# Kernel tuning notes

Hardware: AMD Instinct MI355X
Metric: run time of the kernel (lower is better)

## Reference

```python
import jax, jax.numpy as jnp
from jax import lax
import numpy as np

DEPTH, D_MODEL, D_INNER, D_STATE, DT_RANK = 24, 192, 384, 16, 12
EPS = 1e-5

def _layernorm(x, w, b):
    m = x.mean(-1, keepdims=True)
    v = ((x - m) ** 2).mean(-1, keepdims=True)
    return (x - m) * lax.rsqrt(v + EPS) * w + b

def _silu(x):
    return x * jax.nn.sigmoid(x)

def _mamba_mixer(x, in_w, cw, cb, xp_w, dtw, dtb, a_log, dvec, out_w):
    # x: (B, L, D_MODEL)
    B, L, _ = x.shape
    xz = jnp.einsum('bld,ed->ble', x, in_w)            # (B, L, 2*D_INNER)
    xi, z = xz[..., :D_INNER], xz[..., D_INNER:]
    # causal depthwise conv1d, kernel 4 (left-pad 3, truncate to L)
    xt = jnp.moveaxis(xi, 1, 2)                        # (B, D_INNER, L)
    xt = jnp.pad(xt, ((0, 0), (0, 0), (3, 0)))
    xt = lax.conv_general_dilated(xt, cw[:, None, :], (1,), 'VALID',
                                  dimension_numbers=('NCH', 'OIH', 'NCH'),
                                  feature_group_count=D_INNER)
    xt = _silu(xt + cb[None, :, None])
    xc = jnp.moveaxis(xt, 1, 2)                        # (B, L, D_INNER)
    x_dbl = jnp.einsum('bld,ed->ble', xc, xp_w)        # (B, L, DT_RANK+2*D_STATE)
    dt = x_dbl[..., :DT_RANK]
    Bm = x_dbl[..., DT_RANK:DT_RANK + D_STATE]         # (B, L, N)
    Cm = x_dbl[..., DT_RANK + D_STATE:]                # (B, L, N)
    delta = jax.nn.softplus(jnp.einsum('blr,dr->bld', dt, dtw) + dtb)  # (B, L, D_INNER)
    A = -jnp.exp(a_log)                                # (D_INNER, N)
    dA = jnp.exp(delta[..., None] * A)                 # (B, L, D_INNER, N)
    dBx = (delta * xc)[..., None] * Bm[:, :, None, :]  # (B, L, D_INNER, N)

    def step(h, inp):
        dA_t, dBx_t, C_t = inp
        h = dA_t * h + dBx_t
        y = jnp.einsum('bdn,bn->bd', h, C_t)
        return h, y

    h0 = jnp.zeros((B, D_INNER, D_STATE), x.dtype)
    _, ys = lax.scan(step, h0, (jnp.moveaxis(dA, 1, 0), jnp.moveaxis(dBx, 1, 0), jnp.moveaxis(Cm, 1, 0)))
    y = jnp.moveaxis(ys, 0, 1) + xc * dvec             # (B, L, D_INNER)
    y = y * _silu(z)
    return jnp.einsum('ble,de->bld', y, out_w)

def _forward(x, patch_w, patch_b, norm_w, norm_b, in_proj_w, conv_w, conv_b,
             x_proj_w, dt_w, dt_b, A_log, Dp, out_proj_w, normf_w, normf_b, head_w, head_b):
    # patch embed: conv 16x16 stride 16 -> (B, 192, 14, 14) -> (B, 196, 192)
    h = lax.conv_general_dilated(x, patch_w, (16, 16), 'VALID',
                                 dimension_numbers=('NCHW', 'OIHW', 'NCHW'))
    h = h + patch_b[None, :, None, None]
    B = h.shape[0]
    hidden = h.reshape(B, D_MODEL, -1).transpose(0, 2, 1)  # (B, L, D)
    residual = None
    for d in range(DEPTH):
        residual = hidden if residual is None else residual + hidden
        normed = _layernorm(residual, norm_w[d], norm_b[d])
        hidden = _mamba_mixer(normed, in_proj_w[d], conv_w[d], conv_b[d], x_proj_w[d],
                              dt_w[d], dt_b[d], A_log[d], Dp[d], out_proj_w[d])
    residual = residual + hidden
    feat = _layernorm(residual, normf_w, normf_b)
    pooled = feat.mean(axis=1)                           # final_pool_type='mean'
    return pooled @ head_w.T + head_b                    # (B, num_classes)

def setup_inputs() -> dict:
    key = jax.random.key(0)
    ks = jax.random.split(key, 16)
    s = 0.05
    return {
        'x': jax.random.normal(ks[0], (64, 3, 224, 224), jnp.float32),
        'patch_w': jax.random.normal(ks[1], (192, 3, 16, 16), jnp.float32) * s,
        'patch_b': jnp.zeros((192,), jnp.float32),
        'norm_w': jnp.ones((DEPTH, D_MODEL), jnp.float32),
        'norm_b': jnp.zeros((DEPTH, D_MODEL), jnp.float32),
        'in_proj_w': jax.random.normal(ks[2], (DEPTH, 2 * D_INNER, D_MODEL), jnp.float32) * s,
        'conv_w': jax.random.normal(ks[3], (DEPTH, D_INNER, 4), jnp.float32) * 0.3,
        'conv_b': jnp.zeros((DEPTH, D_INNER), jnp.float32),
        'x_proj_w': jax.random.normal(ks[4], (DEPTH, DT_RANK + 2 * D_STATE, D_INNER), jnp.float32) * s,
        'dt_w': jax.random.normal(ks[5], (DEPTH, D_INNER, DT_RANK), jnp.float32) * s,
        'dt_b': jax.random.uniform(ks[6], (DEPTH, D_INNER), jnp.float32, -4.0, -2.0),
        'A_log': jnp.log(jnp.broadcast_to(jnp.arange(1, D_STATE + 1, dtype=jnp.float32), (DEPTH, D_INNER, D_STATE))),
        'Dp': jnp.ones((DEPTH, D_INNER), jnp.float32),
        'out_proj_w': jax.random.normal(ks[7], (DEPTH, D_MODEL, D_INNER), jnp.float32) * s,
        'normf_w': jnp.ones((D_MODEL,), jnp.float32),
        'normf_b': jnp.zeros((D_MODEL,), jnp.float32),
        'head_w': jax.random.normal(ks[8], (1000, D_MODEL), jnp.float32) * s,
        'head_b': jnp.zeros((1000,), jnp.float32),
    }

def reference(x, patch_w, patch_b, norm_w, norm_b, in_proj_w, conv_w, conv_b,
              x_proj_w, dt_w, dt_b, A_log, Dp, out_proj_w, normf_w, normf_b, head_w, head_b):
    return _forward(x, patch_w, patch_b, norm_w, norm_b, in_proj_w, conv_w, conv_b,
                    x_proj_w, dt_w, dt_b, A_log, Dp, out_proj_w, normf_w, normf_b, head_w, head_b)
```

## Files before the change

kernel.cpp:

```cpp
#include <hip/hip_runtime.h>
#include <math.h>


#define DEPTH 24
#define DM 192
#define DI 384
#define DS 16
#define DR 12
#define SEQL 196
#define BATCH 64
#define MROWS (BATCH*SEQL)
#define XDP 8624
#define LOG2E 1.44269504088896340736f

typedef unsigned short ushort_t;
typedef __bf16 bf16x8 __attribute__((ext_vector_type(8)));
typedef float f32x4 __attribute__((ext_vector_type(4)));

__device__ __forceinline__ float sigmoidf_(float x) { return 1.f / (1.f + __expf(-x)); }

__device__ __forceinline__ ushort_t f2bf(float f) {
    union { float f; unsigned u; } c; c.f = f;
    unsigned u = c.u;
    return (ushort_t)((u + 0x7FFFu + ((u >> 16) & 1u)) >> 16);
}
__device__ __forceinline__ float bf2f(ushort_t u) {
    union { unsigned u; float f; } c; c.u = ((unsigned)u) << 16;
    return c.f;
}

__device__ __forceinline__ void load_lds16(const ushort_t* g, ushort_t* l) {
    __builtin_amdgcn_global_load_lds((__attribute__((address_space(1))) void*)g,
                                     (__attribute__((address_space(3))) void*)l, 16, 0, 0);
}

template<int CTRL>
__device__ __forceinline__ float dpp_mov(float oldv, float src) {
    return __builtin_bit_cast(float, __builtin_amdgcn_update_dpp(
        __builtin_bit_cast(int, oldv), __builtin_bit_cast(int, src),
        CTRL, 0xF, 0xF, false));
}

__device__ __forceinline__ float row16_sum(float v) {
    v += dpp_mov<0xB1>(0.f, v);
    v += dpp_mov<0x4E>(0.f, v);
    v += dpp_mov<0x141>(0.f, v);
    v += dpp_mov<0x140>(0.f, v);
    return v;
}

__global__ void f2bf4_kernel(const float* __restrict__ src, ushort_t* __restrict__ dst, int n4) {
    int i = blockIdx.x * 256 + threadIdx.x;
    if (i >= n4) return;
    float4 v = ((const float4*)src)[i];
    union { ushort_t s[4]; uint2 u; } o;
    o.s[0] = f2bf(v.x); o.s[1] = f2bf(v.y); o.s[2] = f2bf(v.z); o.s[3] = f2bf(v.w);
    ((uint2*)dst)[i] = o.u;
}

__global__ void xp_pad_kernel(const float* __restrict__ src, ushort_t* __restrict__ dst) {
    int i = blockIdx.x * 256 + threadIdx.x;
    if (i >= DEPTH * 64 * 384) return;
    int col = i % 384, row = (i / 384) & 63, d = i / (384 * 64);
    float v = (row < 44) ? src[(size_t)d * 44 * 384 + row * 384 + col] : 0.f;
    dst[i] = f2bf(v);
}

template<bool BF>
__global__ void ln_kernel(float* __restrict__ residual, const float* __restrict__ hidden,
                          const float* __restrict__ w, const float* __restrict__ b,
                          void* __restrict__ out_) {
    int wave = threadIdx.x >> 6, lane = threadIdx.x & 63;
    int row = blockIdx.x * 4 + wave;
    float* rr = residual + (size_t)row * DM;
    const float* hr = hidden + (size_t)row * DM;
    float v0 = rr[lane]       + hr[lane];
    float v1 = rr[lane + 64]  + hr[lane + 64];
    float v2 = rr[lane + 128] + hr[lane + 128];
    rr[lane] = v0; rr[lane + 64] = v1; rr[lane + 128] = v2;
    float s = v0 + v1 + v2;
    #pragma unroll
    for (int off = 32; off > 0; off >>= 1) s += __shfl_down(s, off);
    float mean = __shfl(s, 0) * (1.f / DM);
    float d0 = v0 - mean, d1 = v1 - mean, d2 = v2 - mean;
    float q = d0 * d0 + d1 * d1 + d2 * d2;
    #pragma unroll
    for (int off = 32; off > 0; off >>= 1) q += __shfl_down(q, off);
    float rstd = rsqrtf(__shfl(q, 0) * (1.f / DM) + 1e-5f);
    float o0 = d0 * rstd * w[lane]       + b[lane];
    float o1 = d1 * rstd * w[lane + 64]  + b[lane + 64];
    float o2 = d2 * rstd * w[lane + 128] + b[lane + 128];
    if constexpr (BF) {
        ushort_t* o = (ushort_t*)out_ + (size_t)row * DM;
        o[lane] = f2bf(o0); o[lane + 64] = f2bf(o1); o[lane + 128] = f2bf(o2);
    } else {
        float* o = (float*)out_ + (size_t)row * DM;
        o[lane] = o0; o[lane + 64] = o1; o[lane + 128] = o2;
    }
}

template<int BN, int WM, int WN, int NST, bool TC>
__global__ __launch_bounds__(256, 2) void gemm_mfma(const ushort_t* __restrict__ A,
        const ushort_t* __restrict__ W, float* __restrict__ C, int K, int ldC) {
    constexpr int FM = 128 / (WM * 16);
    constexpr int FN = BN / (WN * 16);
    __shared__ ushort_t sA[128 * 32];
    __shared__ ushort_t sB[BN * 32];
    const int t = threadIdx.x;
    const int wave = t >> 6, lane = t & 63;
    const int lr = lane & 15, lq = lane >> 4;
    const int wr = wave / WN, wc = wave % WN;
    const int m0 = blockIdx.x * 128, n0 = blockIdx.y * BN;
    const int wbase = t & ~63;

    f32x4 acc[FM][FN];
    #pragma unroll
    for (int i = 0; i < FM; i++)
        #pragma unroll
        for (int j = 0; j < FN; j++) acc[i][j] = f32x4{0.f, 0.f, 0.f, 0.f};

    for (int k0 = 0; k0 < K; k0 += 32) {
        __syncthreads();
        #pragma unroll
        for (int c = 0; c < 2; c++) {
            int s = c * 256 + t;
            int row = s >> 2;
            int quad = (s & 3) ^ ((row >> 1) & 3);
            load_lds16(A + (size_t)(m0 + row) * K + k0 + quad * 8,
                       sA + (size_t)(c * 256 + wbase) * 8);
        }
        #pragma unroll
        for (int c = 0; c < BN * 4 / 256; c++) {
            int s = c * 256 + t;
            int row = s >> 2;
            int quad = (s & 3) ^ ((row >> 1) & 3);
            load_lds16(W + (size_t)(n0 + row) * K + k0 + quad * 8,
                       sB + (size_t)(c * 256 + wbase) * 8);
        }
        __syncthreads();
        bf16x8 af[FM], bfr[FN];
        #pragma unroll
        for (int i = 0; i < FM; i++) {
            int row = wr * FM * 16 + i * 16 + lr;
            int slot = (row << 2) | (lq ^ ((row >> 1) & 3));
            af[i] = *(const bf16x8*)&sA[(size_t)slot * 8];
        }
        #pragma unroll
        for (int j = 0; j < FN; j++) {
            int row = wc * FN * 16 + j * 16 + lr;
            int slot = (row << 2) | (lq ^ ((row >> 1) & 3));
            bfr[j] = *(const bf16x8*)&sB[(size_t)slot * 8];
        }
        #pragma unroll
        for (int i = 0; i < FM; i++)
            #pragma unroll
            for (int j = 0; j < FN; j++)
                acc[i][j] = __builtin_amdgcn_mfma_f32_16x16x32_bf16(af[i], bfr[j], acc[i][j], 0, 0, 0);
    }
    int crow0 = m0 + wr * FM * 16 + lq * 4;
    int ccol0 = n0 + wc * FN * 16 + lr;
    if constexpr (TC) {
        #pragma unroll
        for (int i = 0; i < FM; i++) {
            int m = crow0 + i * 16;
            int bb = m / 196, l = m % 196;
            #pragma unroll
            for (int j = 0; j < FN; j++) {
                int col = ccol0 + j * 16;
                if (col < 44) {
                    float4 v = {acc[i][j][0], acc[i][j][1], acc[i][j][2], acc[i][j][3]};
                    *(float4*)(C + (size_t)bb * XDP + (size_t)col * 196 + l) = v;
                }
            }
        }
    } else {
        #pragma unroll
        for (int i = 0; i < FM; i++)
            #pragma unroll
            for (int j = 0; j < FN; j++) {
                if (wc * FN + j >= NST) continue;
                float* cp = C + (size_t)(crow0 + i * 16) * ldC + ccol0 + j * 16;
                #pragma unroll
                for (int r = 0; r < 4; r++) cp[(size_t)r * ldC] = acc[i][j][r];
            }
    }
}

__global__ __launch_bounds__(256, 2) void gemm_patch_mfma(const ushort_t* __restrict__ Xbf,
        const ushort_t* __restrict__ Wbf, const float* __restrict__ bias, float* __restrict__ C) {
    constexpr int FM = 2, FN = 4;
    __shared__ ushort_t sA[128 * 32];
    __shared__ ushort_t sB[64 * 32];
    const int t = threadIdx.x;
    const int wave = t >> 6, lane = t & 63;
    const int lr = lane & 15, lq = lane >> 4;
    const int m0 = blockIdx.x * 128, n0 = blockIdx.y * 64;
    const int wbase = t & ~63;

    const ushort_t* abase[2];
    int aquad[2];
    #pragma unroll
    for (int c = 0; c < 2; c++) {
        int s = c * 256 + t;
        int row = s >> 2;
        aquad[c] = (s & 3) ^ ((row >> 1) & 3);
        int m = m0 + row;
        int b = m / 196, r = m % 196, py = r / 14, px = r % 14;
        abase[c] = Xbf + (size_t)b * 150528 + py * 3584 + px * 16;
    }
    int brow = t >> 2;
    int bquad = (t & 3) ^ ((brow >> 1) & 3);
    const ushort_t* bbase = Wbf + (size_t)(n0 + brow) * 768 + bquad * 8;

    f32x4 acc[FM][FN];
    #pragma unroll
    for (int i = 0; i < FM; i++)
        #pragma unroll
        for (int j = 0; j < FN; j++) acc[i][j] = f32x4{0.f, 0.f, 0.f, 0.f};

    for (int k0 = 0; k0 < 768; k0 += 32) {
        __syncthreads();
        #pragma unroll
        for (int c = 0; c < 2; c++) {
            int k = k0 + aquad[c] * 8;
            int ci = k >> 8, ky = (k >> 4) & 15, kx0 = k & 15;
            load_lds16(abase[c] + ci * 50176 + ky * 224 + kx0,
                       sA + (size_t)(c * 256 + wbase) * 8);
        }
        load_lds16(bbase + k0, sB + (size_t)wbase * 8);
        __syncthreads();
        bf16x8 af[FM], bfr[FN];
        #pragma unroll
        for (int i = 0; i < FM; i++) {
            int row = wave * FM * 16 + i * 16 + lr;
            int slot = (row << 2) | (lq ^ ((row >> 1) & 3));
            af[i] = *(const bf16x8*)&sA[(size_t)slot * 8];
        }
        #pragma unroll
        for (int j = 0; j < FN; j++) {
            int row = j * 16 + lr;
            int slot = (row << 2) | (lq ^ ((row >> 1) & 3));
            bfr[j] = *(const bf16x8*)&sB[(size_t)slot * 8];
        }
        #pragma unroll
        for (int i = 0; i < FM; i++)
            #pragma unroll
            for (int j = 0; j < FN; j++)
                acc[i][j] = __builtin_amdgcn_mfma_f32_16x16x32_bf16(af[i], bfr[j], acc[i][j], 0, 0, 0);
    }
    int crow0 = m0 + wave * FM * 16 + lq * 4;
    int ccol0 = n0 + lr;
    #pragma unroll
    for (int i = 0; i < FM; i++)
        #pragma unroll
        for (int j = 0; j < FN; j++) {
            int col = ccol0 + j * 16;
            float bv = bias[col];
            float* cp = C + (size_t)(crow0 + i * 16) * DM + col;
            #pragma unroll
            for (int r = 0; r < 4; r++) cp[(size_t)r * DM] = acc[i][j][r] + bv;
        }
}

template<bool BIAS>
__global__ __launch_bounds__(256, 2) void gemm64(const float* __restrict__ A,
        const float* __restrict__ W, const float* __restrict__ bias,
        float* __restrict__ C, int M, int N, int K) {
    __shared__ float As[32][68];
    __shared__ float Ws[32][68];
    int t = threadIdx.x;
    int m0 = blockIdx.x * 64, n0 = blockIdx.y * 64;
    int lr = t >> 2, lk = (t & 3) * 4;
    int am = m0 + lr; bool avld = am < M;
    const float* Ap = A + (size_t)(avld ? am : 0) * K + lk;
    int wn = n0 + lr; bool wv = wn < N;
    const float* Wp = W + (size_t)(wv ? wn : 0) * K + lk;
    int tm = (t >> 4) * 4, tn = (t & 15) * 4;
    float acc[4][4];
    #pragma unroll
    for (int i = 0; i < 4; i++)
        #pragma unroll
        for (int j = 0; j < 4; j++) acc[i][j] = 0.f;

    for (int k0 = 0; k0 < K; k0 += 32) {
        float4 a0 = make_float4(0.f, 0.f, 0.f, 0.f), a1 = a0, w0 = a0, w1 = a0;
        if (avld) { a0 = *(const float4*)(Ap + k0); a1 = *(const float4*)(Ap + k0 + 16); }
        if (wv)   { w0 = *(const float4*)(Wp + k0); w1 = *(const float4*)(Wp + k0 + 16); }
        __syncthreads();
        As[lk + 0][lr] = a0.x; As[lk + 1][lr] = a0.y; As[lk + 2][lr] = a0.z; As[lk + 3][lr] = a0.w;
        As[lk + 16][lr] = a1.x; As[lk + 17][lr] = a1.y; As[lk + 18][lr] = a1.z; As[lk + 19][lr] = a1.w;
        Ws[lk + 0][lr] = w0.x; Ws[lk + 1][lr] = w0.y; Ws[lk + 2][lr] = w0.z; Ws[lk + 3][lr] = w0.w;
        Ws[lk + 16][lr] = w1.x; Ws[lk + 17][lr] = w1.y; Ws[lk + 18][lr] = w1.z; Ws[lk + 19][lr] = w1.w;
        __syncthreads();
        #pragma unroll
        for (int kk = 0; kk < 32; kk++) {
            float4 x0 = *(const float4*)&As[kk][tm];
            float4 y0 = *(const float4*)&Ws[kk][tn];
            float av[4] = {x0.x, x0.y, x0.z, x0.w};
            float bv[4] = {y0.x, y0.y, y0.z, y0.w};
            #pragma unroll
            for (int i = 0; i < 4; i++)
                #pragma unroll
                for (int j = 0; j < 4; j++) acc[i][j] = fmaf(av[i], bv[j], acc[i][j]);
        }
    }
    #pragma unroll
    for (int i = 0; i < 4; i++) {
        int m = m0 + tm + i;
        if (m >= M) continue;
        float* cr = C + (size_t)m * N;
        int n = n0 + tn;
        if (n < N) {
            float4 v = {acc[i][0], acc[i][1], acc[i][2], acc[i][3]};
            if (BIAS) { v.x += bias[n]; v.y += bias[n + 1]; v.z += bias[n + 2]; v.w += bias[n + 3]; }
            *(float4*)(cr + n) = v;
        }
    }
}

__global__ void conv_silu_kernel(const float* __restrict__ xz, const float* __restrict__ cw,
                                 const float* __restrict__ cb, ushort_t* __restrict__ xcbf) {
    int idx = blockIdx.x * 256 + threadIdx.x;
    if (idx >= MROWS * DI) return;
    int e = idx % DI; int bl = idx / DI; int l = bl % SEQL; int b = bl / SEQL;
    const float* base = xz + (size_t)(b * SEQL) * 768 + e;
    float w0 = cw[e * 4], w1 = cw[e * 4 + 1], w2 = cw[e * 4 + 2], w3 = cw[e * 4 + 3];
    float acc = cb[e];
    if (l >= 3) acc = fmaf(base[(size_t)(l - 3) * 768], w0, acc);
    if (l >= 2) acc = fmaf(base[(size_t)(l - 2) * 768], w1, acc);
    if (l >= 1) acc = fmaf(base[(size_t)(l - 1) * 768], w2, acc);
    acc = fmaf(base[(size_t)l * 768], w3, acc);
    xcbf[idx] = f2bf(acc * sigmoidf_(acc));
}

__global__ __launch_bounds__(512, 6) void scan_kernel(const float* __restrict__ xdt,
        const ushort_t* __restrict__ xcbf, const float* __restrict__ xz,
        const float* __restrict__ dtw, const float* __restrict__ dtb,
        const float* __restrict__ a_log, const float* __restrict__ Dp, ushort_t* __restrict__ y) {
    __shared__ float sd[44 * 196];
    __shared__ float dls[8][196];
    __shared__ float dus[8][196];
    __shared__ ushort_t xcs[8 * 196];
    const int b = blockIdx.x, eg = blockIdx.y;
    const int tid = threadIdx.x;
    const int wave = tid >> 6, lane = tid & 63;
    const int e = eg * 8 + wave;
    const int n = lane & 15, c = lane >> 4;

    {
        const float4* src4 = (const float4*)(xdt + (size_t)b * XDP);
        float4* sd4 = (float4*)sd;
        for (int i = tid; i < XDP / 4; i += 512) sd4[i] = src4[i];
    }
    float wv = 0.f;
    if (lane < DR) wv = dtw[(size_t)e * DR + lane];
    float4 zr0 = make_float4(0.f, 0.f, 0.f, 0.f), zr1 = zr0;
    if (tid < 196) {
        int l = tid;
        const ushort_t* xp = xcbf + (size_t)(b * SEQL + l) * DI + eg * 8;
        ushort4 xq0 = *(const ushort4*)xp;
        ushort4 xq1 = *(const ushort4*)(xp + 4);
        const float* zp = xz + (size_t)(b * SEQL + l) * 768 + DI + eg * 8;
        zr0 = *(const float4*)zp;
        zr1 = *(const float4*)(zp + 4);
        xcs[0 * 196 + l] = xq0.x; xcs[1 * 196 + l] = xq0.y;
        xcs[2 * 196 + l] = xq0.z; xcs[3 * 196 + l] = xq0.w;
        xcs[4 * 196 + l] = xq1.x; xcs[5 * 196 + l] = xq1.y;
        xcs[6 * 196 + l] = xq1.z; xcs[7 * 196 + l] = xq1.w;
    }
    __syncthreads();

    const float Avn = -__expf(a_log[(size_t)e * DS + n]) * LOG2E;
    const float db = dtb[e];
    const bool act = lane < 49;
    const int lb = act ? lane * 4 : 0;

    if (act) {
        f32x4 dt4 = {db, db, db, db};
        #pragma unroll
        for (int k = 0; k < DR; k++) {
            f32x4 r = *(const f32x4*)&sd[k * 196 + lb];
            dt4 += r * __shfl(wv, k);
        }
        f32x4 d4;
        #pragma unroll
        for (int s = 0; s < 4; s++) {
            float v = dt4[s];
            d4[s] = (v > 20.f) ? v : __logf(1.f + __expf(v));
        }
        ushort4 xcq = *(const ushort4*)&xcs[wave * 196 + lb];
        f32x4 du4 = d4 * f32x4{bf2f(xcq.x), bf2f(xcq.y), bf2f(xcq.z), bf2f(xcq.w)};
        *(f32x4*)&dls[wave][lb] = d4;
        *(f32x4*)&dus[wave][lb] = du4;
    }

    const int t0 = (c == 0) ? 0 : 48 * c + 4;
    const int iters = (c == 0) ? 13 : 12;
    const float* Brow = &sd[(12 + n) * 196];
    const float* Crow = &sd[(28 + n) * 196];
    const float* dlw = dls[wave];
    const float* duw = dus[wave];

    float h = 0.f;
    f32x4 dsum = {0.f, 0.f, 0.f, 0.f};
    for (int i = 0; i < iters; i++) {
        int t = t0 + 4 * i;
        f32x4 dl = *(const f32x4*)&dlw[t];
        f32x4 du = *(const f32x4*)&duw[t];
        f32x4 Bn = *(const f32x4*)&Brow[t];
        dsum += dl;
        #pragma unroll
        for (int s = 0; s < 4; s++) {
            float dA = __builtin_amdgcn_exp2f(dl[s] * Avn);
            h = fmaf(h, dA, du[s] * Bn[s]);
        }
    }
    float P = __builtin_amdgcn_exp2f(Avn * (dsum[0] + dsum[1] + dsum[2] + dsum[3]));

    {
        float hp = __shfl_up(h, 16), pp = __shfl_up(P, 16);
        if (c >= 1) { h = fmaf(P, hp, h); P *= pp; }
        hp = __shfl_up(h, 32); pp = __shfl_up(P, 32);
        if (c >= 2) { h = fmaf(P, hp, h); P *= pp; }
    }
    float hin = __shfl_up(h, 16);
    if (c == 0) hin = 0.f;

    const float Dv = Dp[e];
    ushort_t* xcw = &xcs[wave * 196];
    h = hin;
    for (int i = 0; i < iters; i++) {
        int t = t0 + 4 * i;
        f32x4 dl = *(const f32x4*)&dlw[t];
        f32x4 du = *(const f32x4*)&duw[t];
        f32x4 Bn = *(const f32x4*)&Brow[t];
        f32x4 Cn = *(const f32x4*)&Crow[t];
        f32x4 yp;
        #pragma unroll
        for (int s = 0; s < 4; s++) {
            float dA = __builtin_amdgcn_exp2f(dl[s] * Avn);
            h = fmaf(h, dA, du[s] * Bn[s]);
            yp[s] = h * Cn[s];
        }
        #pragma unroll
        for (int s = 0; s < 4; s++) yp[s] = row16_sum(yp[s]);
        if (n < 4) {
            float ysel = (n == 0) ? yp[0] : (n == 1) ? yp[1] : (n == 2) ? yp[2] : yp[3];
            float xcsel = bf2f(xcw[t + n]);
            xcw[t + n] = f2bf(fmaf(xcsel, Dv, ysel));
        }
    }
    __syncthreads();
    if (tid < 196) {
        int l = tid;
        float zv[8] = {zr0.x, zr0.y, zr0.z, zr0.w, zr1.x, zr1.y, zr1.z, zr1.w};
        union { ushort_t s[8]; ushort4 q[2]; } o;
        #pragma unroll
        for (int k = 0; k < 8; k++) {
            float yv = bf2f(xcs[k * 196 + l]);
            float z = zv[k];
            o.s[k] = f2bf(yv * z * sigmoidf_(z));
        }
        ushort_t* yp = y + (size_t)(b * SEQL + l) * DI + eg * 8;
        *(ushort4*)yp = o.q[0];
        *(ushort4*)(yp + 4) = o.q[1];
    }
}

__global__ void pool_kernel(const float* __restrict__ normed, float* __restrict__ pooled) {
    int b = blockIdx.x, d = threadIdx.x;
    float s = 0.f;
    for (int l = 0; l < SEQL; l++) s += normed[(size_t)(b * SEQL + l) * DM + d];
    pooled[b * DM + d] = s * (1.f / 196.f);
}

extern "C" void kernel_launch(void* const* d_in, const int* in_sizes, int n_in,
                              void* d_out, int out_size, void* d_ws, size_t ws_size,
                              hipStream_t stream) {
    const float* x       = (const float*)d_in[0];
    const float* patch_w = (const float*)d_in[1];
    const float* patch_b = (const float*)d_in[2];
    const float* norm_w  = (const float*)d_in[3];
    const float* norm_b  = (const float*)d_in[4];
    const float* in_w    = (const float*)d_in[5];
    const float* conv_w  = (const float*)d_in[6];
    const float* conv_b  = (const float*)d_in[7];
    const float* xp_w    = (const float*)d_in[8];
    const float* dt_w    = (const float*)d_in[9];
    const float* dt_b    = (const float*)d_in[10];
    const float* A_log   = (const float*)d_in[11];
    const float* Dp      = (const float*)d_in[12];
    const float* out_w   = (const float*)d_in[13];
    const float* normf_w = (const float*)d_in[14];
    const float* normf_b = (const float*)d_in[15];
    const float* head_w  = (const float*)d_in[16];
    const float* head_b  = (const float*)d_in[17];

    float* ws = (float*)d_ws;
    float* residual     = ws;
    float* hidden       = ws + 2408448;
    float* xz           = ws + 4816896;
    ushort_t* xcbf      = (ushort_t*)(ws + 14450688);
    ushort_t* y_bf      = (ushort_t*)(ws + 16859136);
    ushort_t* x_bf      = (ushort_t*)(ws + 14450688);
    ushort_t* normed_bf = (ushort_t*)(ws + 19267584);
    float* xdbl_t       = ws + 20471808;
    float* pooled       = ws + 21023744;
    ushort_t* in_w_bf   = (ushort_t*)(ws + 21036032);
    ushort_t* out_w_bf  = (ushort_t*)(ws + 22805504);
    ushort_t* xp_w_bf   = (ushort_t*)(ws + 23690240);
    ushort_t* patch_w_bf= (ushort_t*)(ws + 23985152);

    (void)hipMemsetAsync(residual, 0, (size_t)2408448 * sizeof(float), stream);

    f2bf4_kernel<<<3456, 256, 0, stream>>>(in_w, in_w_bf, 884736);
    f2bf4_kernel<<<1728, 256, 0, stream>>>(out_w, out_w_bf, 442368);
    f2bf4_kernel<<<144, 256, 0, stream>>>(patch_w, patch_w_bf, 36864);
    f2bf4_kernel<<<9408, 256, 0, stream>>>(x, x_bf, 2408448);
    xp_pad_kernel<<<2304, 256, 0, stream>>>(xp_w, xp_w_bf);

    gemm_patch_mfma<<<dim3(98, 3), 256, 0, stream>>>(x_bf, patch_w_bf, patch_b, hidden);

    for (int d = 0; d < DEPTH; ++d) {
        ln_kernel<true><<<3136, 256, 0, stream>>>(residual, hidden, norm_w + d * DM,
                                                  norm_b + d * DM, normed_bf);
        gemm_mfma<192, 2, 2, 12, false><<<dim3(98, 4), 256, 0, stream>>>(normed_bf,
                in_w_bf + (size_t)d * 768 * 192, xz, 192, 768);
        conv_silu_kernel<<<18816, 256, 0, stream>>>(xz, conv_w + d * DI * 4, conv_b + d * DI, xcbf);
        gemm_mfma<64, 4, 1, 3, true><<<dim3(98, 1), 256, 0, stream>>>(xcbf,
                xp_w_bf + (size_t)d * 64 * 384, xdbl_t, 384, 196);
        scan_kernel<<<dim3(64, 48), 512, 0, stream>>>(xdbl_t, xcbf, xz, dt_w + d * DI * DR,
                dt_b + d * DI, A_log + d * DI * DS, Dp + d * DI, y_bf);
        gemm_mfma<64, 4, 1, 4, false><<<dim3(98, 3), 256, 0, stream>>>(y_bf,
                out_w_bf + (size_t)d * 192 * 384, hidden, 384, 192);
    }

    ln_kernel<false><<<3136, 256, 0, stream>>>(residual, hidden, normf_w, normf_b, xz);
    pool_kernel<<<64, 192, 0, stream>>>(xz, pooled);
    gemm64<true><<<dim3(1, 16), 256, 0, stream>>>(pooled, head_w, head_b, (float*)d_out, 64, 1000, 192);
}
```

Baseline: 3.030 ms.

## Fuse residual add into out_proj GEMM, vectorize conv, shrink GEMM M tiles

Accumulates the out_proj result directly into the residual buffer in the GEMM epilogue. LayerNorm then only reads the residual, which removes the separate hidden buffer, the residual write-back and the initial memset. The causal conv+SiLU kernel now processes four channels per thread with float4 loads. The x_proj and out_proj GEMMs use 64-row tiles to launch twice as many blocks. The read-modify-write epilogue adds a load of C per output element.

```diff
diff --git a/kernel.cpp b/kernel.cpp
--- a/kernel.cpp
+++ b/kernel.cpp
@@ -67,17 +67,15 @@
 }
 
 template<bool BF>
-__global__ void ln_kernel(float* __restrict__ residual, const float* __restrict__ hidden,
+__global__ void ln_kernel(const float* __restrict__ residual,
                           const float* __restrict__ w, const float* __restrict__ b,
                           void* __restrict__ out_) {
     int wave = threadIdx.x >> 6, lane = threadIdx.x & 63;
     int row = blockIdx.x * 4 + wave;
-    float* rr = residual + (size_t)row * DM;
-    const float* hr = hidden + (size_t)row * DM;
-    float v0 = rr[lane]       + hr[lane];
-    float v1 = rr[lane + 64]  + hr[lane + 64];
-    float v2 = rr[lane + 128] + hr[lane + 128];
-    rr[lane] = v0; rr[lane + 64] = v1; rr[lane + 128] = v2;
+    const float* rr = residual + (size_t)row * DM;
+    float v0 = rr[lane];
+    float v1 = rr[lane + 64];
+    float v2 = rr[lane + 128];
     float s = v0 + v1 + v2;
     #pragma unroll
     for (int off = 32; off > 0; off >>= 1) s += __shfl_down(s, off);
@@ -99,18 +97,18 @@
     }
 }
 
-template<int BN, int WM, int WN, int NST, bool TC>
+template<int BM, int BN, int WM, int WN, int NST, bool TC, bool RESADD>
 __global__ __launch_bounds__(256, 2) void gemm_mfma(const ushort_t* __restrict__ A,
         const ushort_t* __restrict__ W, float* __restrict__ C, int K, int ldC) {
-    constexpr int FM = 128 / (WM * 16);
+    constexpr int FM = BM / (WM * 16);
     constexpr int FN = BN / (WN * 16);
-    __shared__ ushort_t sA[128 * 32];
+    __shared__ ushort_t sA[BM * 32];
     __shared__ ushort_t sB[BN * 32];
     const int t = threadIdx.x;
     const int wave = t >> 6, lane = t & 63;
     const int lr = lane & 15, lq = lane >> 4;
     const int wr = wave / WN, wc = wave % WN;
-    const int m0 = blockIdx.x * 128, n0 = blockIdx.y * BN;
+    const int m0 = blockIdx.x * BM, n0 = blockIdx.y * BN;
     const int wbase = t & ~63;
 
     f32x4 acc[FM][FN];
@@ -122,7 +120,7 @@
     for (int k0 = 0; k0 < K; k0 += 32) {
         __syncthreads();
         #pragma unroll
-        for (int c = 0; c < 2; c++) {
+        for (int c = 0; c < BM * 4 / 256; c++) {
             int s = c * 256 + t;
             int row = s >> 2;
             int quad = (s & 3) ^ ((row >> 1) & 3);
@@ -181,7 +179,10 @@
                 if (wc * FN + j >= NST) continue;
                 float* cp = C + (size_t)(crow0 + i * 16) * ldC + ccol0 + j * 16;
                 #pragma unroll
-                for (int r = 0; r < 4; r++) cp[(size_t)r * ldC] = acc[i][j][r];
+                for (int r = 0; r < 4; r++) {
+                    if constexpr (RESADD) cp[(size_t)r * ldC] += acc[i][j][r];
+                    else                  cp[(size_t)r * ldC]  = acc[i][j][r];
+                }
             }
     }
 }
@@ -321,16 +322,34 @@
 __global__ void conv_silu_kernel(const float* __restrict__ xz, const float* __restrict__ cw,
                                  const float* __restrict__ cb, ushort_t* __restrict__ xcbf) {
     int idx = blockIdx.x * 256 + threadIdx.x;
-    if (idx >= MROWS * DI) return;
-    int e = idx % DI; int bl = idx / DI; int l = bl % SEQL; int b = bl / SEQL;
-    const float* base = xz + (size_t)(b * SEQL) * 768 + e;
-    float w0 = cw[e * 4], w1 = cw[e * 4 + 1], w2 = cw[e * 4 + 2], w3 = cw[e * 4 + 3];
-    float acc = cb[e];
-    if (l >= 3) acc = fmaf(base[(size_t)(l - 3) * 768], w0, acc);
-    if (l >= 2) acc = fmaf(base[(size_t)(l - 2) * 768], w1, acc);
-    if (l >= 1) acc = fmaf(base[(size_t)(l - 1) * 768], w2, acc);
-    acc = fmaf(base[(size_t)l * 768], w3, acc);
-    xcbf[idx] = f2bf(acc * sigmoidf_(acc));
+    if (idx >= MROWS * (DI / 4)) return;
+    int eq = idx % (DI / 4); int bl = idx / (DI / 4);
+    int l = bl % SEQL; int b = bl / SEQL;
+    int e4 = eq * 4;
+    const float* base = xz + (size_t)(b * SEQL) * 768 + e4;
+    float4 wa = *(const float4*)(cw + (e4 + 0) * 4);
+    float4 wb = *(const float4*)(cw + (e4 + 1) * 4);
+    float4 wc = *(const float4*)(cw + (e4 + 2) * 4);
+    float4 wd = *(const float4*)(cw + (e4 + 3) * 4);
+    float4 acc = *(const float4*)(cb + e4);
+    if (l >= 3) { float4 xv = *(const float4*)(base + (size_t)(l - 3) * 768);
+        acc.x = fmaf(xv.x, wa.x, acc.x); acc.y = fmaf(xv.y, wb.x, acc.y);
+        acc.z = fmaf(xv.z, wc.x, acc.z); acc.w = fmaf(xv.w, wd.x, acc.w); }
+    if (l >= 2) { float4 xv = *(const float4*)(base + (size_t)(l - 2) * 768);
+        acc.x = fmaf(xv.x, wa.y, acc.x); acc.y = fmaf(xv.y, wb.y, acc.y);
+        acc.z = fmaf(xv.z, wc.y, acc.z); acc.w = fmaf(xv.w, wd.y, acc.w); }
+    if (l >= 1) { float4 xv = *(const float4*)(base + (size_t)(l - 1) * 768);
+        acc.x = fmaf(xv.x, wa.z, acc.x); acc.y = fmaf(xv.y, wb.z, acc.y);
+        acc.z = fmaf(xv.z, wc.z, acc.z); acc.w = fmaf(xv.w, wd.z, acc.w); }
+    { float4 xv = *(const float4*)(base + (size_t)l * 768);
+        acc.x = fmaf(xv.x, wa.w, acc.x); acc.y = fmaf(xv.y, wb.w, acc.y);
+        acc.z = fmaf(xv.z, wc.w, acc.z); acc.w = fmaf(xv.w, wd.w, acc.w); }
+    ushort4 o;
+    o.x = f2bf(acc.x * sigmoidf_(acc.x));
+    o.y = f2bf(acc.y * sigmoidf_(acc.y));
+    o.z = f2bf(acc.z * sigmoidf_(acc.z));
+    o.w = f2bf(acc.w * sigmoidf_(acc.w));
+    *(ushort4*)(xcbf + (size_t)idx * 4) = o;
 }
 
 __global__ __launch_bounds__(512, 6) void scan_kernel(const float* __restrict__ xdt,
@@ -498,7 +517,6 @@
 
     float* ws = (float*)d_ws;
     float* residual     = ws;
-    float* hidden       = ws + 2408448;
     float* xz           = ws + 4816896;
     ushort_t* xcbf      = (ushort_t*)(ws + 14450688);
     ushort_t* y_bf      = (ushort_t*)(ws + 16859136);
@@ -511,31 +529,29 @@
     ushort_t* xp_w_bf   = (ushort_t*)(ws + 23690240);
     ushort_t* patch_w_bf= (ushort_t*)(ws + 23985152);
 
-    (void)hipMemsetAsync(residual, 0, (size_t)2408448 * sizeof(float), stream);
-
     f2bf4_kernel<<<3456, 256, 0, stream>>>(in_w, in_w_bf, 884736);
     f2bf4_kernel<<<1728, 256, 0, stream>>>(out_w, out_w_bf, 442368);
     f2bf4_kernel<<<144, 256, 0, stream>>>(patch_w, patch_w_bf, 36864);
     f2bf4_kernel<<<9408, 256, 0, stream>>>(x, x_bf, 2408448);
     xp_pad_kernel<<<2304, 256, 0, stream>>>(xp_w, xp_w_bf);
 
-    gemm_patch_mfma<<<dim3(98, 3), 256, 0, stream>>>(x_bf, patch_w_bf, patch_b, hidden);
+    gemm_patch_mfma<<<dim3(98, 3), 256, 0, stream>>>(x_bf, patch_w_bf, patch_b, residual);
 
     for (int d = 0; d < DEPTH; ++d) {
-        ln_kernel<true><<<3136, 256, 0, stream>>>(residual, hidden, norm_w + d * DM,
+        ln_kernel<true><<<3136, 256, 0, stream>>>(residual, norm_w + d * DM,
                                                   norm_b + d * DM, normed_bf);
-        gemm_mfma<192, 2, 2, 12, false><<<dim3(98, 4), 256, 0, stream>>>(normed_bf,
+        gemm_mfma<128, 192, 2, 2, 12, false, false><<<dim3(98, 4), 256, 0, stream>>>(normed_bf,
                 in_w_bf + (size_t)d * 768 * 192, xz, 192, 768);
-        conv_silu_kernel<<<18816, 256, 0, stream>>>(xz, conv_w + d * DI * 4, conv_b + d * DI, xcbf);
-        gemm_mfma<64, 4, 1, 3, true><<<dim3(98, 1), 256, 0, stream>>>(xcbf,
+        conv_silu_kernel<<<4704, 256, 0, stream>>>(xz, conv_w + d * DI * 4, conv_b + d * DI, xcbf);
+        gemm_mfma<64, 64, 4, 1, 3, true, false><<<dim3(196, 1), 256, 0, stream>>>(xcbf,
                 xp_w_bf + (size_t)d * 64 * 384, xdbl_t, 384, 196);
         scan_kernel<<<dim3(64, 48), 512, 0, stream>>>(xdbl_t, xcbf, xz, dt_w + d * DI * DR,
                 dt_b + d * DI, A_log + d * DI * DS, Dp + d * DI, y_bf);
-        gemm_mfma<64, 4, 1, 4, false><<<dim3(98, 3), 256, 0, stream>>>(y_bf,
-                out_w_bf + (size_t)d * 192 * 384, hidden, 384, 192);
-    }
-
-    ln_kernel<false><<<3136, 256, 0, stream>>>(residual, hidden, normf_w, normf_b, xz);
+        gemm_mfma<64, 64, 4, 1, 4, false, true><<<dim3(196, 3), 256, 0, stream>>>(y_bf,
+                out_w_bf + (size_t)d * 192 * 384, residual, 384, 192);
+    }
+
+    ln_kernel<false><<<3136, 256, 0, stream>>>(residual, normf_w, normf_b, xz);
     pool_kernel<<<64, 192, 0, stream>>>(xz, pooled);
     gemm64<true><<<dim3(1, 16), 256, 0, stream>>>(pooled, head_w, head_b, (float*)d_out, 64, 1000, 192);
 }
```

New measurement: 2.958 ms. 2.4% less time.
